# Kernel tuning notes

Measured on AMD Instinct MI355X. Metric: run time of the kernel, lower is better.

## Reference

```python
import jax, jax.numpy as jnp
import numpy as np

N_HEADS = 4
N_CLASS = 20
REL_PATTERN = [(5, 3)]
DIF_PATTERN = [(3, 6)]


def im2col(x, ksize, dilation):
    # x: (N,C,H,W) -> (C, ksize*ksize, H*W*N); last dim flattened in (h,w,n) order,
    # matching the torch im2col_indices / permute(1,2,3,0) layout used by the module.
    N, C, H, W = x.shape
    p = (ksize // 2) * dilation
    xp = jnp.pad(x, ((0, 0), (0, 0), (p, p), (p, p)))
    cols = jnp.stack([xp[:, :, fi * dilation:fi * dilation + H, fj * dilation:fj * dilation + W]
                      for fi in range(ksize) for fj in range(ksize)], axis=2)  # (N,C,K2,H,W)
    return cols.transpose(1, 2, 3, 4, 0).reshape(C, ksize * ksize, H * W * N)


def col2im(cols, shape, ksize, dilation):
    # cols: (C*K2, H*W*N) -> scatter-add back to (N,C,H,W) (inverse of im2col).
    N, C, H, W = shape
    p = (ksize // 2) * dilation
    K2 = ksize * ksize
    c = cols.reshape(C, K2, H, W, N).transpose(4, 0, 1, 2, 3)  # (N,C,K2,H,W)
    out = jnp.zeros((N, C, H + 2 * p, W + 2 * p), cols.dtype)
    k = 0
    for fi in range(ksize):
        for fj in range(ksize):
            out = out.at[:, :, fi * dilation:fi * dilation + H, fj * dilation:fj * dilation + W].add(c[:, :, k])
            k += 1
    return out[:, :, p:p + H, p:p + W]


def gap_pred(x, w):
    hm = jnp.einsum('nchw,kc->nhwk', x, w)  # heatmaps
    return hm.reshape(x.shape[0], -1, hm.shape[-1]).mean(1), hm


def make_mask(heatmaps, label):
    N, H, W, _ = heatmaps.shape
    sm = jax.nn.relu(heatmaps)
    m = jnp.take_along_axis(sm, label[:, None, None, None], axis=3)[..., 0]  # (N,H,W)
    mx = jnp.clip(m.reshape(N, -1).max(1), 1.0, None)
    return jax.lax.stop_gradient((m / mx[:, None, None])[:, None])  # (N,1,H,W), detached


def infusion(V, Kc, Qc, ksize, dilation, n_heads):
    N, Dv, H, W = V.shape
    D = Kc.shape[1]
    h_dim, vh_dim, K2 = D // n_heads, Dv // n_heads, ksize * ksize
    L = H * W * N
    Kt = im2col(Kc, ksize, dilation).reshape(n_heads, h_dim, K2, L)
    Qt = Qc.transpose(1, 2, 3, 0).reshape(n_heads, h_dim, L)
    att = jax.nn.softmax(jnp.einsum('ahkl,ahl->akl', Kt, Qt), axis=1)  # softmax over window
    Vt = im2col(V, ksize, dilation).reshape(n_heads, vh_dim, K2, L)
    out = jnp.einsum('avkl,akl->avl', Vt, att).reshape(Dv, H, W, N)
    return out.transpose(3, 0, 1, 2)


def diffusion(V, Kc, Qc, ksize, dilation, mask, n_heads):
    N, Dv, H, W = V.shape
    D = Kc.shape[1]
    h_dim, vh_dim, K2 = D // n_heads, Dv // n_heads, ksize * ksize
    L = H * W * N
    Kt = im2col(Kc, ksize, dilation).reshape(n_heads, h_dim, K2, L)
    Qt = Qc.transpose(1, 2, 3, 0).reshape(n_heads, h_dim, L)
    att = jax.nn.softmax(jnp.einsum('ahkl,ahl->akl', Kt, Qt), axis=1)
    mflat = mask[:, 0].transpose(1, 2, 0).reshape(-1)  # (H*W*N)
    att = att * mflat[None, None, :]
    Vt = V.transpose(1, 2, 3, 0).reshape(n_heads, vh_dim, L)
    Vcols = (Vt[:, :, None, :] * att[:, None, :, :]).reshape(Dv * K2, L)
    return col2im(Vcols, V.shape, ksize, dilation)


def setup_inputs() -> dict:
    key = jax.random.key(0)
    ks = jax.random.split(key, 8)
    N, C, H, W = 4, 256, 64, 64
    return {
        'feats': jax.random.normal(ks[0], (N, C, H, W), jnp.float32),
        'K': jax.random.normal(ks[1], (N, C, H, W), jnp.float32),
        'Q': jax.random.normal(ks[2], (N, C, H, W), jnp.float32),
        'w_gap': jax.random.normal(ks[3], (N_CLASS, C), jnp.float32) * 0.05,
        'w_gap_r': jax.random.normal(ks[4], (N_CLASS, C), jnp.float32) * 0.05,
        'conv_w': jax.random.normal(ks[5], (C, 2 * C, 3, 3), jnp.float32) * 0.02,
        'conv_b': jax.random.normal(ks[6], (C,), jnp.float32) * 0.02,
        'label': jax.random.randint(ks[7], (N,), 0, N_CLASS),
    }


def reference(feats, K, Q, w_gap, w_gap_r, conv_w, conv_b, label):
    pred, hm = gap_pred(feats, w_gap)
    mask = make_mask(hm, label)
    # NOTE: Bayes calls infuse(feats, Q, K, ...) with K/Q swapped vs the Infusion signature.
    feats_r = sum(infusion(feats, Q, K, ksz, dil, N_HEADS) for ksz, dil in REL_PATTERN)
    pred_r, _ = gap_pred(feats_r, w_gap_r)
    feats_d = sum(diffusion(feats, K, Q, ksz, dil, mask, N_HEADS) for ksz, dil in DIF_PATTERN)
    x = jnp.concatenate([feats * mask, feats_d], axis=1)
    nxt = jax.lax.conv_general_dilated(x, conv_w, (1, 1), ((1, 1), (1, 1)),
                                       dimension_numbers=('NCHW', 'OIHW', 'NCHW'))
    nxt = nxt + conv_b[None, :, None, None]
    return nxt, pred, pred_r
```

## Files before the change

kernel.cpp:

```cpp
#include <hip/hip_runtime.h>
#include <hip/hip_bf16.h>

#define N_IMG 4
#define C_CH 256
#define H_DIM 64
#define W_DIM 64
#define HW 4096
#define NCLASS 20
#define NHEADS 4
#define HD 64

typedef __attribute__((ext_vector_type(8))) short short8;
typedef __attribute__((ext_vector_type(4))) float f32x4;

__device__ __forceinline__ ushort f2bf(float f) {
    unsigned u = __float_as_uint(f);
    u += 0x7FFFu + ((u >> 16) & 1u);
    return (ushort)(u >> 16);
}

__global__ __launch_bounds__(256) void k_zero_border(ushort* __restrict__ xinp,
                                                     unsigned* __restrict__ mmax) {
    int b = blockIdx.x;
    if (b == 0 && threadIdx.x < N_IMG) mmax[threadIdx.x] = 0u;
    int n = b / 260, seg = b % 260;
    size_t base;
    if (seg < 66)       base = ((size_t)(n * 66 + 0) * 66 + seg) * 512;
    else if (seg < 132) base = ((size_t)(n * 66 + 65) * 66 + (seg - 66)) * 512;
    else {
        int c = seg - 132;
        int r = 1 + (c >> 1), x = (c & 1) ? 65 : 0;
        base = ((size_t)(n * 66 + r) * 66 + x) * 512;
    }
    ((unsigned*)(xinp + base))[threadIdx.x] = 0u;
}

__global__ __launch_bounds__(256) void k_mask_m(const float* __restrict__ feats,
                         const float* __restrict__ wgap,
                         const int* __restrict__ label,
                         float* __restrict__ mask, unsigned* __restrict__ mmax) {
    int b = blockIdx.x;
    int n = b >> 6, h = b & 63;
    int t = threadIdx.x;
    int w = t & 63, cq = t >> 6;
    __shared__ float wrow[C_CH];
    __shared__ float part[4][64];
    int lab = label[n];
    wrow[t] = wgap[lab * C_CH + t];
    __syncthreads();
    const float* fp = feats + ((size_t)(n * C_CH + cq * 64)) * HW + h * W_DIM + w;
    float acc = 0.f;
    for (int c = 0; c < 64; c++) acc += fp[(size_t)c * HW] * wrow[cq * 64 + c];
    part[cq][w] = acc;
    __syncthreads();
    if (cq == 0) {
        float m = fmaxf(part[0][w] + part[1][w] + part[2][w] + part[3][w], 0.f);
        mask[n * HW + h * W_DIM + w] = m;
        for (int off = 32; off; off >>= 1) m = fmaxf(m, __shfl_down(m, off, 64));
        if (w == 0) atomicMax(&mmax[n], __float_as_uint(m));
    }
}

__global__ void k_plane_sum(const float* __restrict__ x, float* __restrict__ S) {
    int nc = blockIdx.x;
    const float* p = x + (size_t)nc * HW;
    float s = 0.f;
    for (int i = threadIdx.x; i < HW; i += 256) s += p[i];
    __shared__ float red[4];
    for (int off = 32; off; off >>= 1) s += __shfl_down(s, off, 64);
    int wid = threadIdx.x >> 6;
    if ((threadIdx.x & 63) == 0) red[wid] = s;
    __syncthreads();
    if (threadIdx.x == 0) S[nc] = red[0] + red[1] + red[2] + red[3];
}

__global__ void k_pred2(const float* __restrict__ S_f, const float* __restrict__ wg,
                        const float* __restrict__ S_r, const float* __restrict__ wgr,
                        float* __restrict__ out) {
    int idx = threadIdx.x;
    if (idx < N_IMG * NCLASS) {
        int n = idx / NCLASS, k = idx % NCLASS;
        float s = 0.f;
        for (int c = 0; c < C_CH; c++) s += wg[k * C_CH + c] * S_f[n * C_CH + c];
        out[idx] = s * (1.0f / HW);
    } else if (idx < 2 * N_IMG * NCLASS) {
        int j = idx - N_IMG * NCLASS;
        int n = j / NCLASS, k = j % NCLASS;
        float s = 0.f;
        for (int c = 0; c < C_CH; c++) s += wgr[k * C_CH + c] * S_r[n * C_CH + c];
        out[idx] = s * (1.0f / HW);
    }
}

__global__ __launch_bounds__(256) void k_att_inf(
    const float* __restrict__ patch_t,
    const float* __restrict__ center_t,
    float* __restrict__ att) {
    int b = blockIdx.x;
    int n = b >> 6, h = b & 63;
    int a = blockIdx.y;
    int t = threadIdx.x;
    int w = t & 63;
    int kq = t >> 6;
    __shared__ float att_s[25][64];

    int k0 = (kq == 0) ? 0 : (1 + kq * 6);
    int nk = (kq == 0) ? 7 : 6;

    int offc[7]; float msk[7];
#pragma unroll
    for (int j = 0; j < 7; j++) {
        int k = k0 + ((j < nk) ? j : 0);
        int y = h + (k / 5 - 2) * 3, x = w + (k % 5 - 2) * 3;
        bool v = (y >= 0 && y < 64 && x >= 0 && x < 64) && (j < nk);
        offc[j] = v ? y * 64 + x : 0;
        msk[j] = v ? 1.f : 0.f;
    }
    float s[7];
#pragma unroll
    for (int j = 0; j < 7; j++) s[j] = 0.f;

    const float* cp = center_t + ((size_t)(n * C_CH + a * HD)) * HW + h * W_DIM + w;
    const float* pp = patch_t + ((size_t)(n * C_CH + a * HD)) * HW;
    for (int c4 = 0; c4 < 64; c4 += 4) {
        float cen[4];
        float pv[4][7];
#pragma unroll
        for (int u = 0; u < 4; u++)
            cen[u] = cp[(size_t)(c4 + u) * HW];
#pragma unroll
        for (int u = 0; u < 4; u++) {
            const float* pc = pp + (size_t)(c4 + u) * HW;
#pragma unroll
            for (int j = 0; j < 7; j++)
                if (j < nk) pv[u][j] = pc[offc[j]];
        }
#pragma unroll
        for (int u = 0; u < 4; u++)
#pragma unroll
            for (int j = 0; j < 7; j++)
                if (j < nk) s[j] += pv[u][j] * msk[j] * cen[u];
    }
#pragma unroll
    for (int j = 0; j < 7; j++)
        if (j < nk) att_s[k0 + j][w] = s[j];
    __syncthreads();

    if (t < 64) {
        float v[25];
        float mx = -1e30f;
#pragma unroll
        for (int k = 0; k < 25; k++) { v[k] = att_s[k][t]; mx = fmaxf(mx, v[k]); }
        float sum = 0.f;
#pragma unroll
        for (int k = 0; k < 25; k++) { v[k] = __expf(v[k] - mx); sum += v[k]; }
        float inv = 1.0f / sum;
#pragma unroll
        for (int k = 0; k < 25; k++)
            att[((size_t)(a * 25 + k) * N_IMG + n) * HW + h * 64 + t] = v[k] * inv;
    }
}

__global__ __launch_bounds__(256) void k_scatter_w(const float* __restrict__ att,
                                                   float* __restrict__ W) {
    int b = blockIdx.x;
    int n = b >> 6, y = b & 63;
    int t = threadIdx.x;
    int x = t & 63, a = t >> 6;
    float s = 0.f;
#pragma unroll
    for (int k = 0; k < 25; k++) {
        int sy = y - (k / 5 - 2) * 3, sx = x - (k % 5 - 2) * 3;
        if (sy >= 0 && sy < 64 && sx >= 0 && sx < 64)
            s += att[((size_t)(a * 25 + k) * N_IMG + n) * HW + sy * 64 + sx];
    }
    W[((size_t)a * N_IMG + n) * HW + y * 64 + x] = s;
}

__global__ __launch_bounds__(256) void k_wsum(const float* __restrict__ V,
                                              const float* __restrict__ W,
                                              float* __restrict__ S) {
    int nc = blockIdx.x;
    int n = nc >> 8, c = nc & 255;
    int a = c >> 6;
    const f32x4* p4 = (const f32x4*)(V + (size_t)nc * HW);
    const f32x4* w4 = (const f32x4*)(W + ((size_t)a * N_IMG + n) * HW);
    f32x4 a4 = (f32x4){0.f, 0.f, 0.f, 0.f};
    for (int i = threadIdx.x; i < HW / 4; i += 256) {
        f32x4 u = p4[i], v = w4[i];
        a4 += u * v;
    }
    float s = a4[0] + a4[1] + a4[2] + a4[3];
    __shared__ float red[4];
    for (int off = 32; off; off >>= 1) s += __shfl_down(s, off, 64);
    int wid = threadIdx.x >> 6;
    if ((threadIdx.x & 63) == 0) red[wid] = s;
    __syncthreads();
    if (threadIdx.x == 0) S[nc] = red[0] + red[1] + red[2] + red[3];
}

__global__ __launch_bounds__(1024) void k_att_dif(
    const float* __restrict__ patch_t,
    const float* __restrict__ center_t,
    const float* __restrict__ mask, const unsigned* __restrict__ mmax,
    float* __restrict__ att) {
    int b = blockIdx.x;
    int n = b >> 6, h = b & 63;
    int t = threadIdx.x;
    int w = t & 63;
    int a = (t >> 6) & 3;
    int cq = t >> 8;
    __shared__ float att_s[4][9][64];
    for (int i = t; i < 4 * 9 * 64; i += 1024) ((float*)att_s)[i] = 0.f;
    __syncthreads();

    int off[9];
#pragma unroll
    for (int k = 0; k < 9; k++) {
        int y = h + (k / 3 - 1) * 6, x = w + (k % 3 - 1) * 6;
        off[k] = (y >= 0 && y < 64 && x >= 0 && x < 64) ? y * 64 + x : -1;
    }
    float s[9];
#pragma unroll
    for (int k = 0; k < 9; k++) s[k] = 0.f;
    const float* cp = center_t + ((size_t)(n * C_CH + a * HD + cq * 16)) * HW + h * W_DIM + w;
    const float* pp = patch_t + ((size_t)(n * C_CH + a * HD + cq * 16)) * HW;
    for (int c = 0; c < 16; c++) {
        float cen = cp[(size_t)c * HW];
        const float* pc = pp + (size_t)c * HW;
#pragma unroll
        for (int k = 0; k < 9; k++) {
            float pv = (off[k] >= 0) ? pc[off[k]] : 0.f;
            s[k] += pv * cen;
        }
    }
#pragma unroll
    for (int k = 0; k < 9; k++) atomicAdd(&att_s[a][k][w], s[k]);
    __syncthreads();
    if (cq == 0) {
        float v[9];
        float mx = -1e30f;
#pragma unroll
        for (int k = 0; k < 9; k++) { v[k] = att_s[a][k][w]; mx = fmaxf(mx, v[k]); }
        float sum = 0.f;
#pragma unroll
        for (int k = 0; k < 9; k++) { v[k] = __expf(v[k] - mx); sum += v[k]; }
        float mnorm = fmaxf(__uint_as_float(mmax[n]), 1.0f);
        float mm = (mask[n * HW + h * W_DIM + w] / mnorm) / sum;
#pragma unroll
        for (int k = 0; k < 9; k++)
            att[((size_t)(a * 9 + k) * N_IMG + n) * HW + h * W_DIM + w] = v[k] * mm;
    }
}

__global__ __launch_bounds__(256) void k_prep_fused(
    const float* __restrict__ feats, const float* __restrict__ mask,
    const unsigned* __restrict__ mmax,
    const float* __restrict__ att, ushort* __restrict__ xinp) {
    int y = blockIdx.x, n = blockIdx.y, g = blockIdx.z;
    int t = threadIdx.x;
    int x = t & 63, cg = t >> 6;
    __shared__ float ftile[3][32][64];
    __shared__ float att_s[9][64];
    __shared__ ushort sx[64][36];
    short8 pk;
    if (g < 8) {
        int cbase = g * 32 + cg * 8;
        float mnorm = fmaxf(__uint_as_float(mmax[n]), 1.0f);
        float mval = mask[n * HW + y * 64 + x] / mnorm;
        const float* fp = feats + ((size_t)(n * C_CH + cbase)) * HW + y * 64 + x;
        float v[8];
#pragma unroll
        for (int i = 0; i < 8; i++) v[i] = fp[(size_t)i * HW];
#pragma unroll
        for (int i = 0; i < 8; i++) pk[i] = (short)f2bf(v[i] * mval);
    } else {
        int gd = g - 8;
        int a = gd >> 1;
        int cd = gd * 32;
        for (int idx = t; idx < 9 * 64; idx += 256) {
            int k = idx >> 6, w = idx & 63;
            int sy = y - (k / 3 - 1) * 6;
            att_s[k][w] = (sy >= 0 && sy < 64)
                ? att[((size_t)(a * 9 + k) * N_IMG + n) * HW + sy * 64 + w] : 0.f;
        }
        const float* fb = feats + ((size_t)(n * C_CH + cd)) * HW;
#pragma unroll
        for (int i = 0; i < 24; i++) {
            int idx = t + 256 * i;
            int r = idx >> 11, c = (idx >> 6) & 31, xx = idx & 63;
            int ry = y + (r - 1) * 6;
            ((float*)ftile)[idx] = (ry >= 0 && ry < 64)
                ? fb[(size_t)c * HW + ry * 64 + xx] : 0.f;
        }
        __syncthreads();
#pragma unroll
        for (int cl = 0; cl < 8; cl++) {
            int c = cg * 8 + cl;
            float v = 0.f;
#pragma unroll
            for (int k = 0; k < 9; k++) {
                int sxk = x - (k % 3 - 1) * 6;
                if (sxk >= 0 && sxk < 64)
                    v += ftile[2 - k / 3][c][sxk] * att_s[k][sxk];
            }
            pk[cl] = (short)f2bf(v);
        }
    }
    __syncthreads();
    *(short8*)&sx[x][cg * 8] = pk;
    __syncthreads();
    int px = t >> 2, j = t & 3;
    short8 v8 = *(const short8*)&sx[px][j * 8];
    int chb = (g < 8) ? g * 32 : 256 + (g - 8) * 32;
    *(short8*)(xinp + ((size_t)((n * 66 + y + 1) * 66 + px + 1)) * 512 + chb + j * 8) = v8;
}

__global__ __launch_bounds__(256) void k_prep_w(const float* __restrict__ cw,
                                                ushort* __restrict__ wt3) {
    int idx = blockIdx.x * 256 + threadIdx.x;
    int oc = idx >> 9, ic = idx & 511;
    const float* p = cw + (size_t)idx * 9;
    int icc = ic >> 5, lq = (ic & 31) >> 3, pos = ic & 7;
#pragma unroll
    for (int kk = 0; kk < 9; kk++)
        wt3[((((size_t)(icc * 9 + kk)) * 4 + lq) * 256 + oc) * 8 + pos] = f2bf(p[kk]);
}

#define LDS_PXW 32
__global__ __launch_bounds__(512, 4) void k_conv_mfma(
    const ushort* __restrict__ xinp,
    const ushort* __restrict__ wt3,
    const float* __restrict__ cb,
    float* __restrict__ out) {
    int t512 = threadIdx.x;
    int half = t512 >> 8;
    int th   = t512 & 255;
    int lane = t512 & 63;
    int wid  = (t512 >> 6) & 3;
    int bid = blockIdx.x;
    int w   = (bid & 7) * 64 + (bid >> 3);
    int och = w & 1;
    int y0  = (w >> 1) & 63;
    int n   = w >> 7;
    int ocw = och * 128 + wid * 32;
    int l15 = lane & 15, lq = lane >> 4;

    __shared__ ushort lds[2][2][792 * 8];

    f32x4 acc[2][4];
#pragma unroll
    for (int m = 0; m < 2; m++)
#pragma unroll
        for (int xs = 0; xs < 4; xs++) acc[m][xs] = (f32x4){0.f, 0.f, 0.f, 0.f};

    int s0 = th, s1 = th + 256, s2 = th + 512, s3 = th + 768;
    short8 g0, g1, g2, g3;
    int icb = half * 8;

#define SWZ_OFF(R, PX, J) (((((((R) * 66 + (PX)) << 2) | (J)) ^ ((PX) & 7)) << 3))

#define STAGE_LOAD(ICC)                                                              \
    {                                                                                \
        int icc_ = (ICC);                                                            \
        { int r = s0 / 264, rem = s0 % 264, px = rem >> 2, j = rem & 3;              \
          g0 = *(const short8*)(xinp + ((size_t)((n * 66 + y0 + r) * 66 + px)) * 512 \
                                 + icc_ * 32 + j * 8); }                             \
        { int r = s1 / 264, rem = s1 % 264, px = rem >> 2, j = rem & 3;              \
          g1 = *(const short8*)(xinp + ((size_t)((n * 66 + y0 + r) * 66 + px)) * 512 \
                                 + icc_ * 32 + j * 8); }                             \
        { int r = s2 / 264, rem = s2 % 264, px = rem >> 2, j = rem & 3;              \
          g2 = *(const short8*)(xinp + ((size_t)((n * 66 + y0 + r) * 66 + px)) * 512 \
                                 + icc_ * 32 + j * 8); }                             \
        if (s3 < 792) {                                                              \
          int r = s3 / 264, rem = s3 % 264, px = rem >> 2, j = rem & 3;              \
          g3 = *(const short8*)(xinp + ((size_t)((n * 66 + y0 + r) * 66 + px)) * 512 \
                                 + icc_ * 32 + j * 8); }                             \
    }

#define STAGE_WRITE(BUF)                                                             \
    {                                                                                \
        ushort* lb = &lds[half][BUF][0];                                             \
        { int r = s0 / 264, rem = s0 % 264, px = rem >> 2, j = rem & 3;              \
          *(short8*)&lb[SWZ_OFF(r, px, j)] = g0; }                                   \
        { int r = s1 / 264, rem = s1 % 264, px = rem >> 2, j = rem & 3;              \
          *(short8*)&lb[SWZ_OFF(r, px, j)] = g1; }                                   \
        { int r = s2 / 264, rem = s2 % 264, px = rem >> 2, j = rem & 3;              \
          *(short8*)&lb[SWZ_OFF(r, px, j)] = g2; }                                   \
        if (s3 < 792) {                                                              \
          int r = s3 / 264, rem = s3 % 264, px = rem >> 2, j = rem & 3;              \
          *(short8*)&lb[SWZ_OFF(r, px, j)] = g3; }                                   \
    }

    STAGE_LOAD(icb);
    STAGE_WRITE(0);
    __syncthreads();

    int cur = 0;
    for (int it = 0; it < 8; it++) {
        int icc = icb + it;
        if (it < 7) STAGE_LOAD(icc + 1);
        const ushort* lp = &lds[half][cur][0];
        const ushort* am0 = wt3 + (size_t)icc * 73728 + lq * 2048 + (ocw + l15) * 8;
        const ushort* am1 = am0 + 128;
        short8 a0c = *(const short8*)(am0);
        short8 a1c = *(const short8*)(am1);
        short8 a0n = *(const short8*)(am0 + 8192);
        short8 a1n = *(const short8*)(am1 + 8192);
#pragma unroll
        for (int kk = 0; kk < 9; kk++) {
            short8 a0nn, a1nn;
            if (kk < 7) {
                a0nn = *(const short8*)(am0 + (kk + 2) * 8192);
                a1nn = *(const short8*)(am1 + (kk + 2) * 8192);
            }
            int ky = kk / 3, kx = kk % 3;
            int kxl = kx + l15;
            const ushort* lrow = lp + SWZ_OFF(ky, kxl, lq);
            short8 b0 = *(const short8*)(lrow);
            short8 b1 = *(const short8*)(lrow + 16 * LDS_PXW);
            short8 b2 = *(const short8*)(lrow + 32 * LDS_PXW);
            short8 b3 = *(const short8*)(lrow + 48 * LDS_PXW);
            acc[0][0] = __builtin_amdgcn_mfma_f32_16x16x32_bf16(a0c, b0, acc[0][0], 0, 0, 0);
            acc[1][0] = __builtin_amdgcn_mfma_f32_16x16x32_bf16(a1c, b0, acc[1][0], 0, 0, 0);
            acc[0][1] = __builtin_amdgcn_mfma_f32_16x16x32_bf16(a0c, b1, acc[0][1], 0, 0, 0);
            acc[1][1] = __builtin_amdgcn_mfma_f32_16x16x32_bf16(a1c, b1, acc[1][1], 0, 0, 0);
            acc[0][2] = __builtin_amdgcn_mfma_f32_16x16x32_bf16(a0c, b2, acc[0][2], 0, 0, 0);
            acc[1][2] = __builtin_amdgcn_mfma_f32_16x16x32_bf16(a1c, b2, acc[1][2], 0, 0, 0);
            acc[0][3] = __builtin_amdgcn_mfma_f32_16x16x32_bf16(a0c, b3, acc[0][3], 0, 0, 0);
            acc[1][3] = __builtin_amdgcn_mfma_f32_16x16x32_bf16(a1c, b3, acc[1][3], 0, 0, 0);
            a0c = a0n; a1c = a1n; a0n = a0nn; a1n = a1nn;
        }
        if (it < 7) {
            STAGE_WRITE(cur ^ 1);
            __syncthreads();
            cur ^= 1;
        }
    }

    float* red = (float*)&lds[0][0][0];
    __syncthreads();
    if (half == 1) {
#pragma unroll
        for (int m = 0; m < 2; m++)
#pragma unroll
            for (int xs = 0; xs < 4; xs++)
#pragma unroll
                for (int r = 0; r < 4; r++)
                    red[(((m * 4 + xs) * 4) + r) * 256 + th] = acc[m][xs][r];
    }
    __syncthreads();
    if (half == 0) {
#pragma unroll
        for (int m = 0; m < 2; m++) {
#pragma unroll
            for (int r = 0; r < 4; r++) {
                int oc = ocw + m * 16 + lq * 4 + r;
                float bias = cb[oc];
                float* op = out + ((size_t)(n * 256 + oc)) * HW + y0 * 64 + l15;
#pragma unroll
                for (int xs = 0; xs < 4; xs++)
                    op[xs * 16] = acc[m][xs][r] + red[(((m * 4 + xs) * 4) + r) * 256 + th] + bias;
            }
        }
    }
#undef STAGE_LOAD
#undef STAGE_WRITE
#undef SWZ_OFF
}

extern "C" void kernel_launch(void* const* d_in, const int* in_sizes, int n_in,
                              void* d_out, int out_size, void* d_ws, size_t ws_size,
                              hipStream_t stream) {
    const float* feats  = (const float*)d_in[0];
    const float* Kten   = (const float*)d_in[1];
    const float* Qten   = (const float*)d_in[2];
    const float* w_gap  = (const float*)d_in[3];
    const float* w_gapr = (const float*)d_in[4];
    const float* conv_w = (const float*)d_in[5];
    const float* conv_b = (const float*)d_in[6];
    const int*   label  = (const int*)d_in[7];
    float* ob           = (float*)d_out;

    float* ws = (float*)d_ws;
    float*    mask    = ws;
    unsigned* mmax    = (unsigned*)(ws + 16384);
    float*    S_f     = ws + 16384 + 4;
    float*    S_r     = S_f + 1024;
    float*    att_inf = S_r + 1024;
    float*    Wpl     = att_inf + 1638400;
    float*    att_dif = Wpl + 65536;
    ushort*   xinp    = (ushort*)(att_dif + 589824);
    ushort*   wt3     = xinp + 8921088;

    const int NXT = N_IMG * C_CH * HW;

    k_zero_border<<<N_IMG * 260, 256, 0, stream>>>(xinp, mmax);

    k_mask_m<<<N_IMG * H_DIM, 256, 0, stream>>>(feats, w_gap, label, mask, mmax);

    k_plane_sum<<<N_IMG * C_CH, 256, 0, stream>>>(feats, S_f);

    k_att_inf<<<dim3(N_IMG * H_DIM, NHEADS), 256, 0, stream>>>(Qten, Kten, att_inf);
    k_scatter_w<<<N_IMG * H_DIM, 256, 0, stream>>>(att_inf, Wpl);
    k_wsum<<<N_IMG * C_CH, 256, 0, stream>>>(feats, Wpl, S_r);

    k_pred2<<<1, 192, 0, stream>>>(S_f, w_gap, S_r, w_gapr, ob + NXT);

    k_att_dif<<<N_IMG * H_DIM, 1024, 0, stream>>>(Kten, Qten, mask, mmax, att_dif);

    k_prep_w<<<512, 256, 0, stream>>>(conv_w, wt3);
    k_prep_fused<<<dim3(64, 4, 16), 256, 0, stream>>>(feats, mask, mmax, att_dif, xinp);

    k_conv_mfma<<<512, 512, 0, stream>>>(xinp, wt3, conv_b, ob);
}
```

Measured before the change: 174.3 us.

## Merge eleven kernel launches into four phase kernels by dependency level

Groups independent kernels (border zeroing, mask, plane sums, infusion attention, weight prep) into one launch dispatched on block index, then diffusion attention plus scatter, then weighted sums plus input packing, and folds the tiny prediction kernel into the conv launch as an extra block. The mmax reset moves to a memset. This is meant to cut launch overhead and the idle tails between small serial kernels. The cost is branchy kernels that share one shared-memory size and register budget across roles, which can lower occupancy for the lighter roles.

```diff
diff --git a/kernel.cpp b/kernel.cpp
--- a/kernel.cpp
+++ b/kernel.cpp
@@ -19,312 +19,291 @@
     return (ushort)(u >> 16);
 }
 
-__global__ __launch_bounds__(256) void k_zero_border(ushort* __restrict__ xinp,
-                                                     unsigned* __restrict__ mmax) {
-    int b = blockIdx.x;
-    if (b == 0 && threadIdx.x < N_IMG) mmax[threadIdx.x] = 0u;
-    int n = b / 260, seg = b % 260;
-    size_t base;
-    if (seg < 66)       base = ((size_t)(n * 66 + 0) * 66 + seg) * 512;
-    else if (seg < 132) base = ((size_t)(n * 66 + 65) * 66 + (seg - 66)) * 512;
-    else {
-        int c = seg - 132;
-        int r = 1 + (c >> 1), x = (c & 1) ? 65 : 0;
-        base = ((size_t)(n * 66 + r) * 66 + x) * 512;
-    }
-    ((unsigned*)(xinp + base))[threadIdx.x] = 0u;
-}
-
-__global__ __launch_bounds__(256) void k_mask_m(const float* __restrict__ feats,
-                         const float* __restrict__ wgap,
-                         const int* __restrict__ label,
-                         float* __restrict__ mask, unsigned* __restrict__ mmax) {
-    int b = blockIdx.x;
-    int n = b >> 6, h = b & 63;
-    int t = threadIdx.x;
-    int w = t & 63, cq = t >> 6;
-    __shared__ float wrow[C_CH];
-    __shared__ float part[4][64];
-    int lab = label[n];
-    wrow[t] = wgap[lab * C_CH + t];
-    __syncthreads();
-    const float* fp = feats + ((size_t)(n * C_CH + cq * 64)) * HW + h * W_DIM + w;
-    float acc = 0.f;
-    for (int c = 0; c < 64; c++) acc += fp[(size_t)c * HW] * wrow[cq * 64 + c];
-    part[cq][w] = acc;
-    __syncthreads();
-    if (cq == 0) {
-        float m = fmaxf(part[0][w] + part[1][w] + part[2][w] + part[3][w], 0.f);
-        mask[n * HW + h * W_DIM + w] = m;
-        for (int off = 32; off; off >>= 1) m = fmaxf(m, __shfl_down(m, off, 64));
-        if (w == 0) atomicMax(&mmax[n], __float_as_uint(m));
-    }
-}
-
-__global__ void k_plane_sum(const float* __restrict__ x, float* __restrict__ S) {
-    int nc = blockIdx.x;
-    const float* p = x + (size_t)nc * HW;
-    float s = 0.f;
-    for (int i = threadIdx.x; i < HW; i += 256) s += p[i];
-    __shared__ float red[4];
-    for (int off = 32; off; off >>= 1) s += __shfl_down(s, off, 64);
-    int wid = threadIdx.x >> 6;
-    if ((threadIdx.x & 63) == 0) red[wid] = s;
-    __syncthreads();
-    if (threadIdx.x == 0) S[nc] = red[0] + red[1] + red[2] + red[3];
-}
-
-__global__ void k_pred2(const float* __restrict__ S_f, const float* __restrict__ wg,
-                        const float* __restrict__ S_r, const float* __restrict__ wgr,
-                        float* __restrict__ out) {
-    int idx = threadIdx.x;
-    if (idx < N_IMG * NCLASS) {
-        int n = idx / NCLASS, k = idx % NCLASS;
-        float s = 0.f;
-        for (int c = 0; c < C_CH; c++) s += wg[k * C_CH + c] * S_f[n * C_CH + c];
-        out[idx] = s * (1.0f / HW);
-    } else if (idx < 2 * N_IMG * NCLASS) {
-        int j = idx - N_IMG * NCLASS;
-        int n = j / NCLASS, k = j % NCLASS;
-        float s = 0.f;
-        for (int c = 0; c < C_CH; c++) s += wgr[k * C_CH + c] * S_r[n * C_CH + c];
-        out[idx] = s * (1.0f / HW);
-    }
-}
-
-__global__ __launch_bounds__(256) void k_att_inf(
+__global__ __launch_bounds__(256) void k_phaseA(
+    ushort* __restrict__ xinp,
+    const float* __restrict__ feats, const float* __restrict__ wgap,
+    const int* __restrict__ label,
+    float* __restrict__ mask, unsigned* __restrict__ mmax,
+    float* __restrict__ S_f,
     const float* __restrict__ patch_t,
     const float* __restrict__ center_t,
-    float* __restrict__ att) {
+    float* __restrict__ att_inf,
+    const float* __restrict__ cw, ushort* __restrict__ wt3) {
+    __shared__ __align__(16) float smem[1600];
     int b = blockIdx.x;
-    int n = b >> 6, h = b & 63;
-    int a = blockIdx.y;
     int t = threadIdx.x;
-    int w = t & 63;
-    int kq = t >> 6;
-    __shared__ float att_s[25][64];
-
-    int k0 = (kq == 0) ? 0 : (1 + kq * 6);
-    int nk = (kq == 0) ? 7 : 6;
-
-    int offc[7]; float msk[7];
-#pragma unroll
-    for (int j = 0; j < 7; j++) {
-        int k = k0 + ((j < nk) ? j : 0);
-        int y = h + (k / 5 - 2) * 3, x = w + (k % 5 - 2) * 3;
-        bool v = (y >= 0 && y < 64 && x >= 0 && x < 64) && (j < nk);
-        offc[j] = v ? y * 64 + x : 0;
-        msk[j] = v ? 1.f : 0.f;
-    }
-    float s[7];
-#pragma unroll
-    for (int j = 0; j < 7; j++) s[j] = 0.f;
-
-    const float* cp = center_t + ((size_t)(n * C_CH + a * HD)) * HW + h * W_DIM + w;
-    const float* pp = patch_t + ((size_t)(n * C_CH + a * HD)) * HW;
-    for (int c4 = 0; c4 < 64; c4 += 4) {
-        float cen[4];
-        float pv[4][7];
-#pragma unroll
-        for (int u = 0; u < 4; u++)
-            cen[u] = cp[(size_t)(c4 + u) * HW];
-#pragma unroll
-        for (int u = 0; u < 4; u++) {
-            const float* pc = pp + (size_t)(c4 + u) * HW;
-#pragma unroll
-            for (int j = 0; j < 7; j++)
-                if (j < nk) pv[u][j] = pc[offc[j]];
-        }
-#pragma unroll
-        for (int u = 0; u < 4; u++)
-#pragma unroll
-            for (int j = 0; j < 7; j++)
-                if (j < nk) s[j] += pv[u][j] * msk[j] * cen[u];
-    }
-#pragma unroll
-    for (int j = 0; j < 7; j++)
-        if (j < nk) att_s[k0 + j][w] = s[j];
-    __syncthreads();
-
-    if (t < 64) {
-        float v[25];
-        float mx = -1e30f;
-#pragma unroll
-        for (int k = 0; k < 25; k++) { v[k] = att_s[k][t]; mx = fmaxf(mx, v[k]); }
-        float sum = 0.f;
-#pragma unroll
-        for (int k = 0; k < 25; k++) { v[k] = __expf(v[k] - mx); sum += v[k]; }
-        float inv = 1.0f / sum;
-#pragma unroll
-        for (int k = 0; k < 25; k++)
-            att[((size_t)(a * 25 + k) * N_IMG + n) * HW + h * 64 + t] = v[k] * inv;
+
+    if (b < 1040) {
+        int n = b / 260, seg = b % 260;
+        size_t base;
+        if (seg < 66)       base = ((size_t)(n * 66 + 0) * 66 + seg) * 512;
+        else if (seg < 132) base = ((size_t)(n * 66 + 65) * 66 + (seg - 66)) * 512;
+        else {
+            int c = seg - 132;
+            int r = 1 + (c >> 1), x = (c & 1) ? 65 : 0;
+            base = ((size_t)(n * 66 + r) * 66 + x) * 512;
+        }
+        ((unsigned*)(xinp + base))[t] = 0u;
+    } else if (b < 1296) {
+        int bb = b - 1040;
+        int n = bb >> 6, h = bb & 63;
+        int w = t & 63, cq = t >> 6;
+        float* wrow = smem;
+        float* part = smem + 256;
+        int lab = label[n];
+        wrow[t] = wgap[lab * C_CH + t];
+        __syncthreads();
+        const float* fp = feats + ((size_t)(n * C_CH + cq * 64)) * HW + h * W_DIM + w;
+        float acc = 0.f;
+        for (int c = 0; c < 64; c++) acc += fp[(size_t)c * HW] * wrow[cq * 64 + c];
+        part[cq * 64 + w] = acc;
+        __syncthreads();
+        if (cq == 0) {
+            float m = fmaxf(part[w] + part[64 + w] + part[128 + w] + part[192 + w], 0.f);
+            mask[n * HW + h * W_DIM + w] = m;
+            for (int off = 32; off; off >>= 1) m = fmaxf(m, __shfl_down(m, off, 64));
+            if (w == 0) atomicMax(&mmax[n], __float_as_uint(m));
+        }
+    } else if (b < 2320) {
+        int nc = b - 1296;
+        const float* p = feats + (size_t)nc * HW;
+        float s = 0.f;
+        for (int i = t; i < HW; i += 256) s += p[i];
+        float* red = smem;
+        for (int off = 32; off; off >>= 1) s += __shfl_down(s, off, 64);
+        int wid = t >> 6;
+        if ((t & 63) == 0) red[wid] = s;
+        __syncthreads();
+        if (t == 0) S_f[nc] = red[0] + red[1] + red[2] + red[3];
+    } else if (b < 3344) {
+        int idx = b - 2320;
+        int a = idx >> 8;
+        int bb = idx & 255;
+        int n = bb >> 6, h = bb & 63;
+        int w = t & 63;
+        int kq = t >> 6;
+        float* att_s = smem;
+
+        int k0 = (kq == 0) ? 0 : (1 + kq * 6);
+        int nk = (kq == 0) ? 7 : 6;
+        int offc[7]; float msk[7];
+#pragma unroll
+        for (int j = 0; j < 7; j++) {
+            int k = k0 + ((j < nk) ? j : 0);
+            int y = h + (k / 5 - 2) * 3, x = w + (k % 5 - 2) * 3;
+            bool v = (y >= 0 && y < 64 && x >= 0 && x < 64) && (j < nk);
+            offc[j] = v ? y * 64 + x : 0;
+            msk[j] = v ? 1.f : 0.f;
+        }
+        float s[7];
+#pragma unroll
+        for (int j = 0; j < 7; j++) s[j] = 0.f;
+        const float* cp = center_t + ((size_t)(n * C_CH + a * HD)) * HW + h * W_DIM + w;
+        const float* pp = patch_t + ((size_t)(n * C_CH + a * HD)) * HW;
+        for (int c4 = 0; c4 < 64; c4 += 4) {
+            float cen[4];
+            float pv[4][7];
+#pragma unroll
+            for (int u = 0; u < 4; u++)
+                cen[u] = cp[(size_t)(c4 + u) * HW];
+#pragma unroll
+            for (int u = 0; u < 4; u++) {
+                const float* pc = pp + (size_t)(c4 + u) * HW;
+#pragma unroll
+                for (int j = 0; j < 7; j++)
+                    if (j < nk) pv[u][j] = pc[offc[j]];
+            }
+#pragma unroll
+            for (int u = 0; u < 4; u++)
+#pragma unroll
+                for (int j = 0; j < 7; j++)
+                    if (j < nk) s[j] += pv[u][j] * msk[j] * cen[u];
+        }
+#pragma unroll
+        for (int j = 0; j < 7; j++)
+            if (j < nk) att_s[(k0 + j) * 64 + w] = s[j];
+        __syncthreads();
+        if (t < 64) {
+            float v[25];
+            float mx = -1e30f;
+#pragma unroll
+            for (int k = 0; k < 25; k++) { v[k] = att_s[k * 64 + t]; mx = fmaxf(mx, v[k]); }
+            float sum = 0.f;
+#pragma unroll
+            for (int k = 0; k < 25; k++) { v[k] = __expf(v[k] - mx); sum += v[k]; }
+            float inv = 1.0f / sum;
+#pragma unroll
+            for (int k = 0; k < 25; k++)
+                att_inf[((size_t)(a * 25 + k) * N_IMG + n) * HW + h * 64 + t] = v[k] * inv;
+        }
+    } else {
+        int idx = (b - 3344) * 256 + t;
+        const float* p = cw + (size_t)idx * 9;
+        int ic = idx & 511;
+        int oc = idx >> 9;
+        int icc = ic >> 5, lq = (ic & 31) >> 3, pos = ic & 7;
+#pragma unroll
+        for (int kk = 0; kk < 9; kk++)
+            wt3[((((size_t)(icc * 9 + kk)) * 4 + lq) * 256 + oc) * 8 + pos] = f2bf(p[kk]);
     }
 }
 
-__global__ __launch_bounds__(256) void k_scatter_w(const float* __restrict__ att,
-                                                   float* __restrict__ W) {
-    int b = blockIdx.x;
-    int n = b >> 6, y = b & 63;
-    int t = threadIdx.x;
-    int x = t & 63, a = t >> 6;
-    float s = 0.f;
-#pragma unroll
-    for (int k = 0; k < 25; k++) {
-        int sy = y - (k / 5 - 2) * 3, sx = x - (k % 5 - 2) * 3;
-        if (sy >= 0 && sy < 64 && sx >= 0 && sx < 64)
-            s += att[((size_t)(a * 25 + k) * N_IMG + n) * HW + sy * 64 + sx];
-    }
-    W[((size_t)a * N_IMG + n) * HW + y * 64 + x] = s;
-}
-
-__global__ __launch_bounds__(256) void k_wsum(const float* __restrict__ V,
-                                              const float* __restrict__ W,
-                                              float* __restrict__ S) {
-    int nc = blockIdx.x;
-    int n = nc >> 8, c = nc & 255;
-    int a = c >> 6;
-    const f32x4* p4 = (const f32x4*)(V + (size_t)nc * HW);
-    const f32x4* w4 = (const f32x4*)(W + ((size_t)a * N_IMG + n) * HW);
-    f32x4 a4 = (f32x4){0.f, 0.f, 0.f, 0.f};
-    for (int i = threadIdx.x; i < HW / 4; i += 256) {
-        f32x4 u = p4[i], v = w4[i];
-        a4 += u * v;
-    }
-    float s = a4[0] + a4[1] + a4[2] + a4[3];
-    __shared__ float red[4];
-    for (int off = 32; off; off >>= 1) s += __shfl_down(s, off, 64);
-    int wid = threadIdx.x >> 6;
-    if ((threadIdx.x & 63) == 0) red[wid] = s;
-    __syncthreads();
-    if (threadIdx.x == 0) S[nc] = red[0] + red[1] + red[2] + red[3];
-}
-
-__global__ __launch_bounds__(1024) void k_att_dif(
+__global__ __launch_bounds__(1024) void k_phaseB(
     const float* __restrict__ patch_t,
     const float* __restrict__ center_t,
     const float* __restrict__ mask, const unsigned* __restrict__ mmax,
-    float* __restrict__ att) {
+    float* __restrict__ att_dif,
+    const float* __restrict__ att_inf, float* __restrict__ Wpl) {
+    __shared__ float att_s[4][9][64];
     int b = blockIdx.x;
-    int n = b >> 6, h = b & 63;
     int t = threadIdx.x;
-    int w = t & 63;
-    int a = (t >> 6) & 3;
-    int cq = t >> 8;
-    __shared__ float att_s[4][9][64];
-    for (int i = t; i < 4 * 9 * 64; i += 1024) ((float*)att_s)[i] = 0.f;
-    __syncthreads();
-
-    int off[9];
-#pragma unroll
-    for (int k = 0; k < 9; k++) {
-        int y = h + (k / 3 - 1) * 6, x = w + (k % 3 - 1) * 6;
-        off[k] = (y >= 0 && y < 64 && x >= 0 && x < 64) ? y * 64 + x : -1;
-    }
-    float s[9];
-#pragma unroll
-    for (int k = 0; k < 9; k++) s[k] = 0.f;
-    const float* cp = center_t + ((size_t)(n * C_CH + a * HD + cq * 16)) * HW + h * W_DIM + w;
-    const float* pp = patch_t + ((size_t)(n * C_CH + a * HD + cq * 16)) * HW;
-    for (int c = 0; c < 16; c++) {
-        float cen = cp[(size_t)c * HW];
-        const float* pc = pp + (size_t)c * HW;
+
+    if (b < 256) {
+        int n = b >> 6, h = b & 63;
+        int w = t & 63;
+        int a = (t >> 6) & 3;
+        int cq = t >> 8;
+        for (int i = t; i < 4 * 9 * 64; i += 1024) ((float*)att_s)[i] = 0.f;
+        __syncthreads();
+        int off[9];
 #pragma unroll
         for (int k = 0; k < 9; k++) {
-            float pv = (off[k] >= 0) ? pc[off[k]] : 0.f;
-            s[k] += pv * cen;
-        }
-    }
-#pragma unroll
-    for (int k = 0; k < 9; k++) atomicAdd(&att_s[a][k][w], s[k]);
-    __syncthreads();
-    if (cq == 0) {
-        float v[9];
-        float mx = -1e30f;
-#pragma unroll
-        for (int k = 0; k < 9; k++) { v[k] = att_s[a][k][w]; mx = fmaxf(mx, v[k]); }
-        float sum = 0.f;
-#pragma unroll
-        for (int k = 0; k < 9; k++) { v[k] = __expf(v[k] - mx); sum += v[k]; }
-        float mnorm = fmaxf(__uint_as_float(mmax[n]), 1.0f);
-        float mm = (mask[n * HW + h * W_DIM + w] / mnorm) / sum;
-#pragma unroll
-        for (int k = 0; k < 9; k++)
-            att[((size_t)(a * 9 + k) * N_IMG + n) * HW + h * W_DIM + w] = v[k] * mm;
+            int y = h + (k / 3 - 1) * 6, x = w + (k % 3 - 1) * 6;
+            off[k] = (y >= 0 && y < 64 && x >= 0 && x < 64) ? y * 64 + x : -1;
+        }
+        float s[9];
+#pragma unroll
+        for (int k = 0; k < 9; k++) s[k] = 0.f;
+        const float* cp = center_t + ((size_t)(n * C_CH + a * HD + cq * 16)) * HW + h * W_DIM + w;
+        const float* pp = patch_t + ((size_t)(n * C_CH + a * HD + cq * 16)) * HW;
+        for (int c = 0; c < 16; c++) {
+            float cen = cp[(size_t)c * HW];
+            const float* pc = pp + (size_t)c * HW;
+#pragma unroll
+            for (int k = 0; k < 9; k++) {
+                float pv = (off[k] >= 0) ? pc[off[k]] : 0.f;
+                s[k] += pv * cen;
+            }
+        }
+#pragma unroll
+        for (int k = 0; k < 9; k++) atomicAdd(&att_s[a][k][w], s[k]);
+        __syncthreads();
+        if (cq == 0) {
+            float v[9];
+            float mx = -1e30f;
+#pragma unroll
+            for (int k = 0; k < 9; k++) { v[k] = att_s[a][k][w]; mx = fmaxf(mx, v[k]); }
+            float sum = 0.f;
+#pragma unroll
+            for (int k = 0; k < 9; k++) { v[k] = __expf(v[k] - mx); sum += v[k]; }
+            float mnorm = fmaxf(__uint_as_float(mmax[n]), 1.0f);
+            float mm = (mask[n * HW + h * W_DIM + w] / mnorm) / sum;
+#pragma unroll
+            for (int k = 0; k < 9; k++)
+                att_dif[((size_t)(a * 9 + k) * N_IMG + n) * HW + h * W_DIM + w] = v[k] * mm;
+        }
+    } else {
+        int b2 = b - 256;
+        int x = t & 63, a = (t >> 6) & 3, yl = t >> 8;
+        int row = b2 * 4 + yl;
+        int n = row >> 6, y = row & 63;
+        float s = 0.f;
+#pragma unroll
+        for (int k = 0; k < 25; k++) {
+            int sy = y - (k / 5 - 2) * 3, sx = x - (k % 5 - 2) * 3;
+            if (sy >= 0 && sy < 64 && sx >= 0 && sx < 64)
+                s += att_inf[((size_t)(a * 25 + k) * N_IMG + n) * HW + sy * 64 + sx];
+        }
+        Wpl[((size_t)a * N_IMG + n) * HW + y * 64 + x] = s;
     }
 }
 
-__global__ __launch_bounds__(256) void k_prep_fused(
-    const float* __restrict__ feats, const float* __restrict__ mask,
-    const unsigned* __restrict__ mmax,
+__global__ __launch_bounds__(256) void k_phaseC(
+    const float* __restrict__ feats, const float* __restrict__ Wpl,
+    float* __restrict__ S_r,
+    const float* __restrict__ mask, const unsigned* __restrict__ mmax,
     const float* __restrict__ att, ushort* __restrict__ xinp) {
-    int y = blockIdx.x, n = blockIdx.y, g = blockIdx.z;
+    __shared__ __align__(16) char smemc[31488];
+    int b = blockIdx.x;
     int t = threadIdx.x;
-    int x = t & 63, cg = t >> 6;
-    __shared__ float ftile[3][32][64];
-    __shared__ float att_s[9][64];
-    __shared__ ushort sx[64][36];
-    short8 pk;
-    if (g < 8) {
-        int cbase = g * 32 + cg * 8;
-        float mnorm = fmaxf(__uint_as_float(mmax[n]), 1.0f);
-        float mval = mask[n * HW + y * 64 + x] / mnorm;
-        const float* fp = feats + ((size_t)(n * C_CH + cbase)) * HW + y * 64 + x;
-        float v[8];
-#pragma unroll
-        for (int i = 0; i < 8; i++) v[i] = fp[(size_t)i * HW];
-#pragma unroll
-        for (int i = 0; i < 8; i++) pk[i] = (short)f2bf(v[i] * mval);
+
+    if (b < 1024) {
+        int nc = b;
+        int n = nc >> 8, c = nc & 255;
+        int a = c >> 6;
+        const f32x4* p4 = (const f32x4*)(feats + (size_t)nc * HW);
+        const f32x4* w4 = (const f32x4*)(Wpl + ((size_t)a * N_IMG + n) * HW);
+        f32x4 a4 = (f32x4){0.f, 0.f, 0.f, 0.f};
+        for (int i = t; i < HW / 4; i += 256) {
+            f32x4 u = p4[i], v = w4[i];
+            a4 += u * v;
+        }
+        float s = a4[0] + a4[1] + a4[2] + a4[3];
+        float* red = (float*)smemc;
+        for (int off = 32; off; off >>= 1) s += __shfl_down(s, off, 64);
+        int wid = t >> 6;
+        if ((t & 63) == 0) red[wid] = s;
+        __syncthreads();
+        if (t == 0) S_r[nc] = red[0] + red[1] + red[2] + red[3];
     } else {
-        int gd = g - 8;
-        int a = gd >> 1;
-        int cd = gd * 32;
-        for (int idx = t; idx < 9 * 64; idx += 256) {
-            int k = idx >> 6, w = idx & 63;
-            int sy = y - (k / 3 - 1) * 6;
-            att_s[k][w] = (sy >= 0 && sy < 64)
-                ? att[((size_t)(a * 9 + k) * N_IMG + n) * HW + sy * 64 + w] : 0.f;
-        }
-        const float* fb = feats + ((size_t)(n * C_CH + cd)) * HW;
-#pragma unroll
-        for (int i = 0; i < 24; i++) {
-            int idx = t + 256 * i;
-            int r = idx >> 11, c = (idx >> 6) & 31, xx = idx & 63;
-            int ry = y + (r - 1) * 6;
-            ((float*)ftile)[idx] = (ry >= 0 && ry < 64)
-                ? fb[(size_t)c * HW + ry * 64 + xx] : 0.f;
-        }
-        __syncthreads();
-#pragma unroll
-        for (int cl = 0; cl < 8; cl++) {
-            int c = cg * 8 + cl;
-            float v = 0.f;
-#pragma unroll
-            for (int k = 0; k < 9; k++) {
-                int sxk = x - (k % 3 - 1) * 6;
-                if (sxk >= 0 && sxk < 64)
-                    v += ftile[2 - k / 3][c][sxk] * att_s[k][sxk];
-            }
-            pk[cl] = (short)f2bf(v);
-        }
-    }
-    __syncthreads();
-    *(short8*)&sx[x][cg * 8] = pk;
-    __syncthreads();
-    int px = t >> 2, j = t & 3;
-    short8 v8 = *(const short8*)&sx[px][j * 8];
-    int chb = (g < 8) ? g * 32 : 256 + (g - 8) * 32;
-    *(short8*)(xinp + ((size_t)((n * 66 + y + 1) * 66 + px + 1)) * 512 + chb + j * 8) = v8;
-}
-
-__global__ __launch_bounds__(256) void k_prep_w(const float* __restrict__ cw,
-                                                ushort* __restrict__ wt3) {
-    int idx = blockIdx.x * 256 + threadIdx.x;
-    int oc = idx >> 9, ic = idx & 511;
-    const float* p = cw + (size_t)idx * 9;
-    int icc = ic >> 5, lq = (ic & 31) >> 3, pos = ic & 7;
-#pragma unroll
-    for (int kk = 0; kk < 9; kk++)
-        wt3[((((size_t)(icc * 9 + kk)) * 4 + lq) * 256 + oc) * 8 + pos] = f2bf(p[kk]);
+        int idx = b - 1024;
+        int y = idx & 63, n = (idx >> 6) & 3, g = idx >> 8;
+        int x = t & 63, cg = t >> 6;
+        float (*ftile)[32][64] = (float(*)[32][64])smemc;
+        float (*att_s)[64]     = (float(*)[64])(smemc + 24576);
+        ushort (*sx)[36]       = (ushort(*)[36])(smemc + 26880);
+        short8 pk;
+        if (g < 8) {
+            int cbase = g * 32 + cg * 8;
+            float mnorm = fmaxf(__uint_as_float(mmax[n]), 1.0f);
+            float mval = mask[n * HW + y * 64 + x] / mnorm;
+            const float* fp = feats + ((size_t)(n * C_CH + cbase)) * HW + y * 64 + x;
+            float v[8];
+#pragma unroll
+            for (int i = 0; i < 8; i++) v[i] = fp[(size_t)i * HW];
+#pragma unroll
+            for (int i = 0; i < 8; i++) pk[i] = (short)f2bf(v[i] * mval);
+        } else {
+            int gd = g - 8;
+            int a = gd >> 1;
+            int cd = gd * 32;
+            for (int idx2 = t; idx2 < 9 * 64; idx2 += 256) {
+                int k = idx2 >> 6, w = idx2 & 63;
+                int sy = y - (k / 3 - 1) * 6;
+                att_s[k][w] = (sy >= 0 && sy < 64)
+                    ? att[((size_t)(a * 9 + k) * N_IMG + n) * HW + sy * 64 + w] : 0.f;
+            }
+            const float* fb = feats + ((size_t)(n * C_CH + cd)) * HW;
+#pragma unroll
+            for (int i = 0; i < 24; i++) {
+                int idx2 = t + 256 * i;
+                int r = idx2 >> 11, c = (idx2 >> 6) & 31, xx = idx2 & 63;
+                int ry = y + (r - 1) * 6;
+                ((float*)ftile)[idx2] = (ry >= 0 && ry < 64)
+                    ? fb[(size_t)c * HW + ry * 64 + xx] : 0.f;
+            }
+            __syncthreads();
+#pragma unroll
+            for (int cl = 0; cl < 8; cl++) {
+                int c = cg * 8 + cl;
+                float v = 0.f;
+#pragma unroll
+                for (int k = 0; k < 9; k++) {
+                    int sxk = x - (k % 3 - 1) * 6;
+                    if (sxk >= 0 && sxk < 64)
+                        v += ftile[2 - k / 3][c][sxk] * att_s[k][sxk];
+                }
+                pk[cl] = (short)f2bf(v);
+            }
+        }
+        __syncthreads();
+        *(short8*)&sx[x][cg * 8] = pk;
+        __syncthreads();
+        int px = t >> 2, j = t & 3;
+        short8 v8 = *(const short8*)&sx[px][j * 8];
+        int chb = (g < 8) ? g * 32 : 256 + (g - 8) * 32;
+        *(short8*)(xinp + ((size_t)((n * 66 + y + 1) * 66 + px + 1)) * 512 + chb + j * 8) = v8;
+    }
 }
 
 #define LDS_PXW 32
@@ -332,13 +311,32 @@
     const ushort* __restrict__ xinp,
     const ushort* __restrict__ wt3,
     const float* __restrict__ cb,
-    float* __restrict__ out) {
+    float* __restrict__ out,
+    const float* __restrict__ S_f, const float* __restrict__ wg,
+    const float* __restrict__ S_r, const float* __restrict__ wgr,
+    float* __restrict__ pred_out) {
+    int bid = blockIdx.x;
+    if (bid == 512) {
+        int idx = threadIdx.x;
+        if (idx < N_IMG * NCLASS) {
+            int n = idx / NCLASS, k = idx % NCLASS;
+            float s = 0.f;
+            for (int c = 0; c < C_CH; c++) s += wg[k * C_CH + c] * S_f[n * C_CH + c];
+            pred_out[idx] = s * (1.0f / HW);
+        } else if (idx < 2 * N_IMG * NCLASS) {
+            int j = idx - N_IMG * NCLASS;
+            int n = j / NCLASS, k = j % NCLASS;
+            float s = 0.f;
+            for (int c = 0; c < C_CH; c++) s += wgr[k * C_CH + c] * S_r[n * C_CH + c];
+            pred_out[idx] = s * (1.0f / HW);
+        }
+        return;
+    }
     int t512 = threadIdx.x;
     int half = t512 >> 8;
     int th   = t512 & 255;
     int lane = t512 & 63;
     int wid  = (t512 >> 6) & 3;
-    int bid = blockIdx.x;
     int w   = (bid & 7) * 64 + (bid >> 3);
     int och = w & 1;
     int y0  = (w >> 1) & 63;
@@ -495,22 +493,14 @@
 
     const int NXT = N_IMG * C_CH * HW;
 
-    k_zero_border<<<N_IMG * 260, 256, 0, stream>>>(xinp, mmax);
-
-    k_mask_m<<<N_IMG * H_DIM, 256, 0, stream>>>(feats, w_gap, label, mask, mmax);
-
-    k_plane_sum<<<N_IMG * C_CH, 256, 0, stream>>>(feats, S_f);
-
-    k_att_inf<<<dim3(N_IMG * H_DIM, NHEADS), 256, 0, stream>>>(Qten, Kten, att_inf);
-    k_scatter_w<<<N_IMG * H_DIM, 256, 0, stream>>>(att_inf, Wpl);
-    k_wsum<<<N_IMG * C_CH, 256, 0, stream>>>(feats, Wpl, S_r);
-
-    k_pred2<<<1, 192, 0, stream>>>(S_f, w_gap, S_r, w_gapr, ob + NXT);
-
-    k_att_dif<<<N_IMG * H_DIM, 1024, 0, stream>>>(Kten, Qten, mask, mmax, att_dif);
-
-    k_prep_w<<<512, 256, 0, stream>>>(conv_w, wt3);
-    k_prep_fused<<<dim3(64, 4, 16), 256, 0, stream>>>(feats, mask, mmax, att_dif, xinp);
-
-    k_conv_mfma<<<512, 512, 0, stream>>>(xinp, wt3, conv_b, ob);
+    hipMemsetAsync(mmax, 0, N_IMG * sizeof(unsigned), stream);
+
+    k_phaseA<<<3856, 256, 0, stream>>>(xinp, feats, w_gap, label, mask, mmax,
+                                       S_f, Qten, Kten, att_inf, conv_w, wt3);
+    k_phaseB<<<320, 1024, 0, stream>>>(Kten, Qten, mask, mmax, att_dif,
+                                       att_inf, Wpl);
+    k_phaseC<<<5120, 256, 0, stream>>>(feats, Wpl, S_r, mask, mmax, att_dif, xinp);
+
+    k_conv_mfma<<<513, 512, 0, stream>>>(xinp, wt3, conv_b, ob,
+                                         S_f, w_gap, S_r, w_gapr, ob + NXT);
 }
```

After: 148.9 us. -14.6%, faster.
